# Kernel optimization log

Hardware: AMD Instinct MI355X
Metric: run time of the kernel (lower is better)

## Reference

```python
import jax, jax.numpy as jnp
import numpy as np

N = 100000          # nodes
E = 3200000         # edges (before self-loops)
F_IN = 745
HID = 128
N_CLS = 8
NEG_SLOPE = 0.2
EPS = 1e-16  # PyG softmax epsilon


def gat_conv(x, W, a_src, a_dst, b, src, dst):
    """Single-head GATConv (PyG semantics, self-loops already in src/dst)."""
    h = x @ W                                   # [N, out]
    s_src = h @ a_src                           # [N] per-node source logit
    s_dst = h @ a_dst                           # [N] per-node dest logit
    e = jax.nn.leaky_relu(s_src[src] + s_dst[dst], NEG_SLOPE)  # [E']
    # numerically stable per-destination softmax
    m = jax.ops.segment_max(e, dst, num_segments=N)
    e = jnp.exp(e - m[dst])
    denom = jax.ops.segment_sum(e, dst, num_segments=N)
    alpha = e / (denom[dst] + EPS)              # [E']
    out = jax.ops.segment_sum(alpha[:, None] * h[src], dst, num_segments=N)
    return out + b


def setup_inputs() -> dict:
    key = jax.random.key(0)
    ks = jax.random.split(key, 10)
    x = jax.random.normal(ks[0], (N, F_IN), dtype=jnp.float32)
    edge_index = jax.random.randint(ks[1], (2, E), 0, N, dtype=jnp.int64)
    # layer 1 params (Glorot-ish scale)
    W1 = jax.random.normal(ks[2], (F_IN, HID), dtype=jnp.float32) * (1.0 / np.sqrt(F_IN))
    a1_src = jax.random.normal(ks[3], (HID,), dtype=jnp.float32) * (1.0 / np.sqrt(HID))
    a1_dst = jax.random.normal(ks[4], (HID,), dtype=jnp.float32) * (1.0 / np.sqrt(HID))
    b1 = jnp.zeros((HID,), dtype=jnp.float32)
    # layer 2 params
    W2 = jax.random.normal(ks[5], (HID, N_CLS), dtype=jnp.float32) * (1.0 / np.sqrt(HID))
    a2_src = jax.random.normal(ks[6], (N_CLS,), dtype=jnp.float32) * (1.0 / np.sqrt(N_CLS))
    a2_dst = jax.random.normal(ks[7], (N_CLS,), dtype=jnp.float32) * (1.0 / np.sqrt(N_CLS))
    b2 = jnp.zeros((N_CLS,), dtype=jnp.float32)
    return {"x": x, "edge_index": edge_index, "W1": W1, "a1_src": a1_src,
            "a1_dst": a1_dst, "b1": b1, "W2": W2, "a2_src": a2_src,
            "a2_dst": a2_dst, "b2": b2}


def reference(x, edge_index, W1, a1_src, a1_dst, b1, W2, a2_src, a2_dst, b2):
    # add self-loops (PyG GATConv default add_self_loops=True)
    loop = jnp.arange(N, dtype=edge_index.dtype)
    src = jnp.concatenate([edge_index[0], loop])
    dst = jnp.concatenate([edge_index[1], loop])
    h = gat_conv(x, W1, a1_src, a1_dst, b1, src, dst)
    h = jax.nn.relu(h)
    # dropout p=0.5 is identity in eval mode
    out = gat_conv(h, W2, a2_src, a2_dst, b2, src, dst)
    return out
```

## Files before the change

### kernel.cpp

```cpp
#include <hip/hip_runtime.h>
#include <stdint.h>

#define NN 100000
#define EE 3200000
#define NEDGE (EE + NN)
#define KD 745
#define GKP 768
#define HD 128
#define NC 8

#define BS 256
#define NBK 391
#define NBLK 784
#define CHUNK ((NEDGE + NBLK - 1) / NBLK)

typedef unsigned short ushort_t;
typedef __attribute__((ext_vector_type(8))) short short8;
typedef __attribute__((ext_vector_type(4))) float f32x4;

__device__ __forceinline__ ushort_t f2bf(float f) {
  unsigned int u = __float_as_uint(f);
  u += 0x7FFFu + ((u >> 16) & 1u);
  return (ushort_t)(u >> 16);
}
__device__ __forceinline__ float bf2f(ushort_t h) {
  return __uint_as_float(((unsigned int)h) << 16);
}
__device__ __forceinline__ float lrelu_exp(float t) {
  return __expf(t >= 0.f ? t : 0.2f * t);
}

__global__ void k_detect(const int* __restrict__ ei, int* __restrict__ flag) {
  if (threadIdx.x == 0) {
    int orv = 0;
    #pragma unroll
    for (int i = 0; i < 16; i++) orv |= ei[2 * i + 1];
    flag[0] = (orv == 0) ? 1 : 0;
  }
}

__device__ __forceinline__ void edge_sd(const int* __restrict__ ei, int flag, int e,
                                        int& s, int& d) {
  if (e < EE) {
    if (flag) {
      s = ((const int2*)ei)[e].x;
      d = ((const int2*)ei)[EE + e].x;
    } else {
      s = ei[e];
      d = ei[EE + e];
    }
  } else { s = e - EE; d = s; }
}

__global__ __launch_bounds__(256)
void k_prepw1(const float* __restrict__ W1, ushort_t* __restrict__ WhiT,
              ushort_t* __restrict__ WloT) {
  int idx = blockIdx.x * 256 + threadIdx.x;
  if (idx >= HD * GKP) return;
  int n = idx / GKP, k = idx % GKP;
  float v = (k < KD) ? W1[(size_t)k * HD + n] : 0.f;
  ushort_t hi = f2bf(v);
  ushort_t lo = f2bf(v - bf2f(hi));
  WhiT[(size_t)n * GKP + k] = hi;
  WloT[(size_t)n * GKP + k] = lo;
}

__global__ __launch_bounds__(256, 2)
void k_gemm1(const float* __restrict__ x, const ushort_t* __restrict__ WhiT,
             const ushort_t* __restrict__ WloT, float* __restrict__ h1) {
  __shared__ ushort_t Ah[128 * 32], Al[128 * 32], Bh[128 * 32], Bl[128 * 32];
  const int tid = threadIdx.x;
  const int lane = tid & 63;
  const int wid = tid >> 6;
  const int wr = wid >> 1, wc = wid & 1;
  const long long row0 = (long long)blockIdx.x * 128;
  const int am = tid >> 1, ah = tid & 1;

  f32x4 acc[4][4];
  #pragma unroll
  for (int i = 0; i < 4; i++)
    #pragma unroll
    for (int j = 0; j < 4; j++) acc[i][j] = (f32x4){0.f, 0.f, 0.f, 0.f};

  for (int k0 = 0; k0 < GKP; k0 += 32) {
    {
      long long gr = row0 + am;
      int kb = k0 + ah * 16;
      float v[16];
      if (gr < NN && kb + 16 <= KD) {
        const float* xp = x + gr * KD + kb;
        #pragma unroll
        for (int i = 0; i < 16; i++) v[i] = xp[i];
      } else if (gr < NN) {
        const float* xp = x + gr * KD + kb;
        #pragma unroll
        for (int i = 0; i < 16; i++) v[i] = (kb + i < KD) ? xp[i] : 0.f;
      } else {
        #pragma unroll
        for (int i = 0; i < 16; i++) v[i] = 0.f;
      }
      ushort_t* ph = &Ah[am * 32 + ah * 16];
      ushort_t* pl = &Al[am * 32 + ah * 16];
      #pragma unroll
      for (int i = 0; i < 16; i++) {
        ushort_t hi = f2bf(v[i]);
        ph[i] = hi;
        pl[i] = f2bf(v[i] - bf2f(hi));
      }
    }
    {
      const int bn = tid >> 1, off = (tid & 1) * 16;
      const ushort_t* gh = WhiT + (size_t)bn * GKP + k0 + off;
      const ushort_t* gl = WloT + (size_t)bn * GKP + k0 + off;
      ushort_t* dh = &Bh[bn * 32 + off];
      ushort_t* dl = &Bl[bn * 32 + off];
      *(short8*)dh = *(const short8*)gh;
      *(short8*)(dh + 8) = *(const short8*)(gh + 8);
      *(short8*)dl = *(const short8*)gl;
      *(short8*)(dl + 8) = *(const short8*)(gl + 8);
    }
    __syncthreads();

    const int rr = lane & 15, kk = (lane >> 4) * 8;
    short8 a_h[4], a_l[4], b_h[4], b_l[4];
    #pragma unroll
    for (int i = 0; i < 4; i++) {
      a_h[i] = *(const short8*)&Ah[(wr * 64 + i * 16 + rr) * 32 + kk];
      a_l[i] = *(const short8*)&Al[(wr * 64 + i * 16 + rr) * 32 + kk];
      b_h[i] = *(const short8*)&Bh[(wc * 64 + i * 16 + rr) * 32 + kk];
      b_l[i] = *(const short8*)&Bl[(wc * 64 + i * 16 + rr) * 32 + kk];
    }
    #pragma unroll
    for (int i = 0; i < 4; i++)
      #pragma unroll
      for (int j = 0; j < 4; j++) {
        acc[i][j] = __builtin_amdgcn_mfma_f32_16x16x32_bf16(a_h[i], b_h[j], acc[i][j], 0, 0, 0);
        acc[i][j] = __builtin_amdgcn_mfma_f32_16x16x32_bf16(a_h[i], b_l[j], acc[i][j], 0, 0, 0);
        acc[i][j] = __builtin_amdgcn_mfma_f32_16x16x32_bf16(a_l[i], b_h[j], acc[i][j], 0, 0, 0);
      }
    __syncthreads();
  }
  #pragma unroll
  for (int i = 0; i < 4; i++)
    #pragma unroll
    for (int j = 0; j < 4; j++)
      #pragma unroll
      for (int r = 0; r < 4; r++) {
        long long grow = row0 + wr * 64 + i * 16 + (lane >> 4) * 4 + r;
        int gcol = wc * 64 + j * 16 + (lane & 15);
        if (grow < NN) h1[grow * HD + gcol] = acc[i][j][r];
      }
}

__global__ __launch_bounds__(256)
void k_s1(const float* __restrict__ h1, const float* __restrict__ as_,
          const float* __restrict__ ad_, float* __restrict__ s1s,
          float* __restrict__ s1d) {
  int w = threadIdx.x >> 6, lane = threadIdx.x & 63;
  int n = blockIdx.x * 4 + w;
  if (n >= NN) return;
  const float* hp = h1 + (size_t)n * HD;
  float h0 = hp[lane], h1v = hp[lane + 64];
  float ps = h0 * as_[lane] + h1v * as_[lane + 64];
  float pd = h0 * ad_[lane] + h1v * ad_[lane + 64];
  #pragma unroll
  for (int m = 32; m; m >>= 1) {
    ps += __shfl_xor(ps, m, 64);
    pd += __shfl_xor(pd, m, 64);
  }
  if (lane == 0) { s1s[n] = ps; s1d[n] = pd; }
}

__global__ __launch_bounds__(256)
void k_hist(const int* __restrict__ ei, const int* __restrict__ flagp,
            int* __restrict__ hist) {
  __shared__ int cnt[NBK];
  const int flag = flagp[0];
  int b = blockIdx.x, t = threadIdx.x;
  for (int i = t; i < NBK; i += 256) cnt[i] = 0;
  __syncthreads();
  int e0 = b * CHUNK;
  int e1 = e0 + CHUNK; if (e1 > NEDGE) e1 = NEDGE;
  for (int e = e0 + t; e < e1; e += 256) {
    int s, d;
    edge_sd(ei, flag, e, s, d);
    atomicAdd(&cnt[d >> 8], 1);
  }
  __syncthreads();
  for (int i = t; i < NBK; i += 256) hist[(size_t)i * NBLK + b] = cnt[i];
}

__global__ __launch_bounds__(256)
void k_scanA(int* __restrict__ hist, int* __restrict__ btot) {
  __shared__ int sm[1024];
  int j = blockIdx.x, t = threadIdx.x;
  #pragma unroll
  for (int c = 0; c < 4; c++) {
    int i = t + 256 * c;
    sm[i] = (i < NBLK) ? hist[(size_t)j * NBLK + i] : 0;
  }
  __syncthreads();
  for (int d = 1; d < 1024; d <<= 1) {
    int v[4];
    #pragma unroll
    for (int c = 0; c < 4; c++) {
      int i = t + 256 * c;
      v[c] = (i >= d) ? sm[i - d] : 0;
    }
    __syncthreads();
    #pragma unroll
    for (int c = 0; c < 4; c++) sm[t + 256 * c] += v[c];
    __syncthreads();
  }
  #pragma unroll
  for (int c = 0; c < 4; c++) {
    int i = t + 256 * c;
    if (i < NBLK) hist[(size_t)j * NBLK + i] = (i == 0) ? 0 : sm[i - 1];
  }
  if (t == 0) btot[j] = sm[NBLK - 1];
}

__global__ __launch_bounds__(256)
void k_bscan(const int* __restrict__ btot, int* __restrict__ bbase) {
  __shared__ int sm[512];
  int t = threadIdx.x;
  for (int i = t; i < 512; i += 256) sm[i] = (i < NBK) ? btot[i] : 0;
  __syncthreads();
  for (int d = 1; d < 512; d <<= 1) {
    int v0 = (t >= d) ? sm[t - d] : 0;
    int v1 = sm[t + 256 - d];
    __syncthreads();
    sm[t] += v0;
    sm[t + 256] += v1;
    __syncthreads();
  }
  for (int i = t; i <= NBK; i += 256) bbase[i] = (i == 0) ? 0 : sm[i - 1];
}

__global__ __launch_bounds__(256)
void k_place(const int* __restrict__ ei, const int* __restrict__ flagp,
             const int* __restrict__ hist, const int* __restrict__ bbase,
             int* __restrict__ pairs) {
  __shared__ int ofs[NBK];
  const int flag = flagp[0];
  int b = blockIdx.x, t = threadIdx.x;
  for (int i = t; i < NBK; i += 256)
    ofs[i] = bbase[i] + hist[(size_t)i * NBLK + b];
  __syncthreads();
  int e0 = b * CHUNK;
  int e1 = e0 + CHUNK; if (e1 > NEDGE) e1 = NEDGE;
  for (int e = e0 + t; e < e1; e += 256) {
    int s, d;
    edge_sd(ei, flag, e, s, d);
    int pos = atomicAdd(&ofs[d >> 8], 1);
    pairs[pos] = s | ((d & 255) << 17);
  }
}

__global__ __launch_bounds__(256)
void k_part2(const int* __restrict__ pairs, const int* __restrict__ bbase,
             int* __restrict__ rp, int* __restrict__ adj) {
  __shared__ int cnt[BS], fillv[BS], wsum[4];
  int b = blockIdx.x, t = threadIdx.x;
  int n0 = b * BS;
  int j0 = bbase[b];
  int ne = bbase[b + 1] - j0;
  const int* pb = pairs + j0;
  cnt[t] = 0;
  __syncthreads();
  for (int j = t; j < ne; j += 256)
    atomicAdd(&cnt[((unsigned)pb[j]) >> 17], 1);
  __syncthreads();
  int lane = t & 63, w = t >> 6;
  int v = cnt[t];
  int xv = v;
  #pragma unroll
  for (int d = 1; d < 64; d <<= 1) {
    int y = __shfl_up(xv, d, 64);
    if (lane >= d) xv += y;
  }
  if (lane == 63) wsum[w] = xv;
  __syncthreads();
  int woff = 0;
  #pragma unroll
  for (int i = 0; i < 4; i++) if (i < w) woff += wsum[i];
  int excl = j0 + woff + xv - v;
  if (n0 + t < NN) rp[n0 + t] = excl;
  fillv[t] = excl;
  __syncthreads();
  for (int j = t; j < ne; j += 256) {
    int p = pb[j];
    int pos = atomicAdd(&fillv[((unsigned)p) >> 17], 1);
    adj[pos] = p & 0x1FFFF;
  }
  if (b == 0 && t == 0) rp[NN] = NEDGE;
}

__global__ __launch_bounds__(256)
void k_agg1h2(const float* __restrict__ h1, const int* __restrict__ adj,
              const int* __restrict__ rp, const float* __restrict__ s1s,
              const float* __restrict__ s1d, const float* __restrict__ b1,
              const float* __restrict__ W2, const float* __restrict__ a2s,
              const float* __restrict__ a2d, float* __restrict__ h2,
              float* __restrict__ s2s, float* __restrict__ s2d) {
  __shared__ float W2T[NC * HD];
  int t = threadIdx.x;
  for (int i = t; i < HD * NC; i += 256) {
    int f = i >> 3, k = i & 7;
    W2T[k * HD + f] = W2[i];
  }
  __syncthreads();
  int wv = t >> 6, lane = t & 63;
  int n = blockIdx.x * 4 + wv;
  if (n >= NN) return;
  int half = lane >> 5, l32 = lane & 31;
  int j0 = rp[n], j1 = rp[n + 1];
  int deg = j1 - j0;
  int dh = (deg + 1) >> 1;
  int js = half ? (j0 + dh) : j0;
  int je = half ? j1 : (j0 + dh);
  float sdv = s1d[n];
  f32x4 acc = (f32x4){0.f, 0.f, 0.f, 0.f};
  float dsum = 0.f;
  int j = js;
  for (; j + 4 <= je; j += 4) {
    int e0 = adj[j], e1 = adj[j + 1], e2 = adj[j + 2], e3 = adj[j + 3];
    f32x4 v0 = *(const f32x4*)(h1 + (size_t)e0 * HD + l32 * 4);
    f32x4 v1 = *(const f32x4*)(h1 + (size_t)e1 * HD + l32 * 4);
    f32x4 v2 = *(const f32x4*)(h1 + (size_t)e2 * HD + l32 * 4);
    f32x4 v3 = *(const f32x4*)(h1 + (size_t)e3 * HD + l32 * 4);
    float w0 = lrelu_exp(s1s[e0] + sdv);
    float w1 = lrelu_exp(s1s[e1] + sdv);
    float w2 = lrelu_exp(s1s[e2] + sdv);
    float w3 = lrelu_exp(s1s[e3] + sdv);
    acc += w0 * v0; acc += w1 * v1; acc += w2 * v2; acc += w3 * v3;
    dsum += (w0 + w1) + (w2 + w3);
  }
  for (; j < je; ++j) {
    int e0 = adj[j];
    f32x4 v0 = *(const f32x4*)(h1 + (size_t)e0 * HD + l32 * 4);
    float w0 = lrelu_exp(s1s[e0] + sdv);
    acc += w0 * v0; dsum += w0;
  }
  #pragma unroll
  for (int c = 0; c < 4; c++) acc[c] += __shfl_xor(acc[c], 32, 64);
  dsum += __shfl_xor(dsum, 32, 64);
  float inv = 1.f / (dsum + 1e-16f);
  f32x4 bv = *(const f32x4*)(b1 + l32 * 4);
  f32x4 x2v;
  #pragma unroll
  for (int c = 0; c < 4; c++) {
    float r = acc[c] * inv + bv[c];
    x2v[c] = r > 0.f ? r : 0.f;
  }
  float hk[NC];
  #pragma unroll
  for (int k = 0; k < NC; k++) {
    f32x4 wv4 = *(const f32x4*)&W2T[k * HD + l32 * 4];
    hk[k] = x2v[0] * wv4[0] + x2v[1] * wv4[1] + x2v[2] * wv4[2] + x2v[3] * wv4[3];
  }
  #pragma unroll
  for (int m = 1; m < 32; m <<= 1)
    #pragma unroll
    for (int k = 0; k < NC; k++) hk[k] += __shfl_xor(hk[k], m, 64);
  if (lane == 0) {
    float ss = 0.f, sd = 0.f;
    #pragma unroll
    for (int k = 0; k < NC; k++) {
      h2[(size_t)n * NC + k] = hk[k];
      ss += hk[k] * a2s[k];
      sd += hk[k] * a2d[k];
    }
    s2s[n] = ss;
    s2d[n] = sd;
  }
}

__global__ __launch_bounds__(256)
void k_agg2(const float* __restrict__ h2, const int* __restrict__ adj,
            const int* __restrict__ rp, const float* __restrict__ s2s,
            const float* __restrict__ s2d, const float* __restrict__ b2,
            float* __restrict__ out) {
  int wv = threadIdx.x >> 6, lane = threadIdx.x & 63;
  int n = blockIdx.x * 4 + wv;
  if (n >= NN) return;
  int sub = lane >> 3, k = lane & 7;
  int j0 = rp[n], j1 = rp[n + 1];
  float sdv = s2d[n];
  float a = 0.f, dsum = 0.f;
  for (int j = j0 + sub; j < j1; j += 8) {
    int s = adj[j];
    float wvv = lrelu_exp(s2s[s] + sdv);
    a += wvv * h2[(size_t)s * NC + k];
    dsum += wvv;
  }
  #pragma unroll
  for (int m = 8; m < 64; m <<= 1) {
    a += __shfl_xor(a, m, 64);
    dsum += __shfl_xor(dsum, m, 64);
  }
  if (sub == 0) out[(size_t)n * NC + k] = a / (dsum + 1e-16f) + b2[k];
}

extern "C" void kernel_launch(void* const* d_in, const int* in_sizes, int n_in,
                              void* d_out, int out_size, void* d_ws, size_t ws_size,
                              hipStream_t stream) {
  (void)in_sizes; (void)n_in; (void)out_size;
  const float* x   = (const float*)d_in[0];
  const int*   ei  = (const int*)d_in[1];
  const float* W1  = (const float*)d_in[2];
  const float* a1s = (const float*)d_in[3];
  const float* a1d = (const float*)d_in[4];
  const float* b1  = (const float*)d_in[5];
  const float* W2  = (const float*)d_in[6];
  const float* a2s = (const float*)d_in[7];
  const float* a2d = (const float*)d_in[8];
  const float* b2  = (const float*)d_in[9];
  float* out = (float*)d_out;
  char* ws = (char*)d_ws;

  size_t o = 0;
  auto take = [&](size_t bytes) { size_t c = o; o += (bytes + 255) & ~(size_t)255; return c; };
  size_t o_flag  = take(64);
  size_t o_whi   = take((size_t)HD * GKP * 2);
  size_t o_wlo   = take((size_t)HD * GKP * 2);
  size_t o_h1    = take((size_t)NN * HD * 4);
  size_t o_h2    = take((size_t)NN * NC * 4);
  size_t o_s1s   = take((size_t)NN * 4);
  size_t o_s1d   = take((size_t)NN * 4);
  size_t o_s2s   = take((size_t)NN * 4);
  size_t o_s2d   = take((size_t)NN * 4);
  size_t o_rp    = take((size_t)(NN + 1) * 4);
  size_t o_adj   = take((size_t)NEDGE * 4);
  size_t o_pairs = take((size_t)NEDGE * 4);
  size_t o_hist  = take((size_t)NBK * NBLK * 4);
  size_t o_btot  = take((size_t)NBK * 4);
  size_t o_bbase = take((size_t)(NBK + 1) * 4);
  if (o > ws_size) return;

  int*   flag = (int*)(ws + o_flag);
  ushort_t* whi = (ushort_t*)(ws + o_whi);
  ushort_t* wlo = (ushort_t*)(ws + o_wlo);
  float* h1  = (float*)(ws + o_h1);
  float* h2  = (float*)(ws + o_h2);
  float* s1s = (float*)(ws + o_s1s);
  float* s1d = (float*)(ws + o_s1d);
  float* s2s = (float*)(ws + o_s2s);
  float* s2d = (float*)(ws + o_s2d);
  int* rp    = (int*)(ws + o_rp);
  int* adj   = (int*)(ws + o_adj);
  int* pairs = (int*)(ws + o_pairs);
  int* hist  = (int*)(ws + o_hist);
  int* btot  = (int*)(ws + o_btot);
  int* bbase = (int*)(ws + o_bbase);

  k_detect<<<1, 64, 0, stream>>>(ei, flag);
  k_prepw1<<<(HD * GKP + 255) / 256, 256, 0, stream>>>(W1, whi, wlo);
  k_gemm1<<<(NN + 127) / 128, 256, 0, stream>>>(x, whi, wlo, h1);
  k_s1<<<(NN + 3) / 4, 256, 0, stream>>>(h1, a1s, a1d, s1s, s1d);
  k_hist<<<NBLK, 256, 0, stream>>>(ei, flag, hist);
  k_scanA<<<NBK, 256, 0, stream>>>(hist, btot);
  k_bscan<<<1, 256, 0, stream>>>(btot, bbase);
  k_place<<<NBLK, 256, 0, stream>>>(ei, flag, hist, bbase, pairs);
  k_part2<<<NBK, 256, 0, stream>>>(pairs, bbase, rp, adj);
  k_agg1h2<<<(NN + 3) / 4, 256, 0, stream>>>(h1, adj, rp, s1s, s1d, b1, W2,
                                             a2s, a2d, h2, s2s, s2d);
  k_agg2<<<(NN + 3) / 4, 256, 0, stream>>>(h2, adj, rp, s2s, s2d, b2, out);
}
```

Baseline: 891.4 us.

## Store h1 as bf16, fuse attention logits into GEMM epilogue

```diff
diff --git a/kernel.cpp b/kernel.cpp
--- a/kernel.cpp
+++ b/kernel.cpp
@@ -8,6 +8,7 @@
 #define GKP 768
 #define HD 128
 #define NC 8
+#define HDP 132
 
 #define BS 256
 #define NBK 391
@@ -17,6 +18,7 @@
 typedef unsigned short ushort_t;
 typedef __attribute__((ext_vector_type(8))) short short8;
 typedef __attribute__((ext_vector_type(4))) float f32x4;
+typedef __attribute__((ext_vector_type(4))) ushort_t ushort4_t;
 
 __device__ __forceinline__ ushort_t f2bf(float f) {
   unsigned int u = __float_as_uint(f);
@@ -67,8 +69,11 @@
 
 __global__ __launch_bounds__(256, 2)
 void k_gemm1(const float* __restrict__ x, const ushort_t* __restrict__ WhiT,
-             const ushort_t* __restrict__ WloT, float* __restrict__ h1) {
+             const ushort_t* __restrict__ WloT, const float* __restrict__ a1s,
+             const float* __restrict__ a1d, ushort_t* __restrict__ h1b,
+             float* __restrict__ s1s, float* __restrict__ s1d) {
   __shared__ ushort_t Ah[128 * 32], Al[128 * 32], Bh[128 * 32], Bl[128 * 32];
+  __shared__ float sred[128][4];
   const int tid = threadIdx.x;
   const int lane = tid & 63;
   const int wid = tid >> 6;
@@ -140,35 +145,47 @@
       }
     __syncthreads();
   }
+
+  const int cl = lane & 15, gq = lane >> 4;
+  float avS[4], avD[4];
+  #pragma unroll
+  for (int j = 0; j < 4; j++) {
+    avS[j] = a1s[wc * 64 + j * 16 + cl];
+    avD[j] = a1d[wc * 64 + j * 16 + cl];
+  }
   #pragma unroll
   for (int i = 0; i < 4; i++)
     #pragma unroll
-    for (int j = 0; j < 4; j++)
+    for (int r = 0; r < 4; r++) {
+      long long grow = row0 + wr * 64 + i * 16 + gq * 4 + r;
+      float ps = 0.f, pd = 0.f;
       #pragma unroll
-      for (int r = 0; r < 4; r++) {
-        long long grow = row0 + wr * 64 + i * 16 + (lane >> 4) * 4 + r;
-        int gcol = wc * 64 + j * 16 + (lane & 15);
-        if (grow < NN) h1[grow * HD + gcol] = acc[i][j][r];
-      }
-}
-
-__global__ __launch_bounds__(256)
-void k_s1(const float* __restrict__ h1, const float* __restrict__ as_,
-          const float* __restrict__ ad_, float* __restrict__ s1s,
-          float* __restrict__ s1d) {
-  int w = threadIdx.x >> 6, lane = threadIdx.x & 63;
-  int n = blockIdx.x * 4 + w;
-  if (n >= NN) return;
-  const float* hp = h1 + (size_t)n * HD;
-  float h0 = hp[lane], h1v = hp[lane + 64];
-  float ps = h0 * as_[lane] + h1v * as_[lane + 64];
-  float pd = h0 * ad_[lane] + h1v * ad_[lane + 64];
-  #pragma unroll
-  for (int m = 32; m; m >>= 1) {
-    ps += __shfl_xor(ps, m, 64);
-    pd += __shfl_xor(pd, m, 64);
-  }
-  if (lane == 0) { s1s[n] = ps; s1d[n] = pd; }
+      for (int j = 0; j < 4; j++) {
+        float hv = acc[i][j][r];
+        ps += hv * avS[j];
+        pd += hv * avD[j];
+        if (grow < NN)
+          h1b[grow * HD + wc * 64 + j * 16 + cl] = f2bf(hv);
+      }
+      #pragma unroll
+      for (int m = 1; m < 16; m <<= 1) {
+        ps += __shfl_xor(ps, m, 64);
+        pd += __shfl_xor(pd, m, 64);
+      }
+      if (cl == 0) {
+        int lrow = wr * 64 + i * 16 + gq * 4 + r;
+        sred[lrow][wc] = ps;
+        sred[lrow][2 + wc] = pd;
+      }
+    }
+  __syncthreads();
+  if (tid < 128) {
+    long long grow = row0 + tid;
+    if (grow < NN) {
+      s1s[grow] = sred[tid][0] + sred[tid][1];
+      s1d[grow] = sred[tid][2] + sred[tid][3];
+    }
+  }
 }
 
 __global__ __launch_bounds__(256)
@@ -297,17 +314,17 @@
 }
 
 __global__ __launch_bounds__(256)
-void k_agg1h2(const float* __restrict__ h1, const int* __restrict__ adj,
+void k_agg1h2(const ushort_t* __restrict__ h1b, const int* __restrict__ adj,
               const int* __restrict__ rp, const float* __restrict__ s1s,
               const float* __restrict__ s1d, const float* __restrict__ b1,
               const float* __restrict__ W2, const float* __restrict__ a2s,
               const float* __restrict__ a2d, float* __restrict__ h2,
               float* __restrict__ s2s, float* __restrict__ s2d) {
-  __shared__ float W2T[NC * HD];
+  __shared__ float W2T[NC * HDP];
   int t = threadIdx.x;
   for (int i = t; i < HD * NC; i += 256) {
     int f = i >> 3, k = i & 7;
-    W2T[k * HD + f] = W2[i];
+    W2T[k * HDP + f] = W2[i];
   }
   __syncthreads();
   int wv = t >> 6, lane = t & 63;
@@ -323,24 +340,35 @@
   f32x4 acc = (f32x4){0.f, 0.f, 0.f, 0.f};
   float dsum = 0.f;
   int j = js;
-  for (; j + 4 <= je; j += 4) {
-    int e0 = adj[j], e1 = adj[j + 1], e2 = adj[j + 2], e3 = adj[j + 3];
-    f32x4 v0 = *(const f32x4*)(h1 + (size_t)e0 * HD + l32 * 4);
-    f32x4 v1 = *(const f32x4*)(h1 + (size_t)e1 * HD + l32 * 4);
-    f32x4 v2 = *(const f32x4*)(h1 + (size_t)e2 * HD + l32 * 4);
-    f32x4 v3 = *(const f32x4*)(h1 + (size_t)e3 * HD + l32 * 4);
-    float w0 = lrelu_exp(s1s[e0] + sdv);
-    float w1 = lrelu_exp(s1s[e1] + sdv);
-    float w2 = lrelu_exp(s1s[e2] + sdv);
-    float w3 = lrelu_exp(s1s[e3] + sdv);
-    acc += w0 * v0; acc += w1 * v1; acc += w2 * v2; acc += w3 * v3;
-    dsum += (w0 + w1) + (w2 + w3);
+  for (; j + 8 <= je; j += 8) {
+    int e[8];
+    ushort4_t u[8];
+    float w[8];
+    #pragma unroll
+    for (int q = 0; q < 8; q++) e[q] = adj[j + q];
+    #pragma unroll
+    for (int q = 0; q < 8; q++)
+      u[q] = *(const ushort4_t*)(h1b + (size_t)e[q] * HD + l32 * 4);
+    #pragma unroll
+    for (int q = 0; q < 8; q++) w[q] = lrelu_exp(s1s[e[q]] + sdv);
+    #pragma unroll
+    for (int q = 0; q < 8; q++) {
+      acc[0] += w[q] * bf2f(u[q][0]);
+      acc[1] += w[q] * bf2f(u[q][1]);
+      acc[2] += w[q] * bf2f(u[q][2]);
+      acc[3] += w[q] * bf2f(u[q][3]);
+      dsum += w[q];
+    }
   }
   for (; j < je; ++j) {
     int e0 = adj[j];
-    f32x4 v0 = *(const f32x4*)(h1 + (size_t)e0 * HD + l32 * 4);
+    ushort4_t u = *(const ushort4_t*)(h1b + (size_t)e0 * HD + l32 * 4);
     float w0 = lrelu_exp(s1s[e0] + sdv);
-    acc += w0 * v0; dsum += w0;
+    acc[0] += w0 * bf2f(u[0]);
+    acc[1] += w0 * bf2f(u[1]);
+    acc[2] += w0 * bf2f(u[2]);
+    acc[3] += w0 * bf2f(u[3]);
+    dsum += w0;
   }
   #pragma unroll
   for (int c = 0; c < 4; c++) acc[c] += __shfl_xor(acc[c], 32, 64);
@@ -356,8 +384,8 @@
   float hk[NC];
   #pragma unroll
   for (int k = 0; k < NC; k++) {
-    f32x4 wv4 = *(const f32x4*)&W2T[k * HD + l32 * 4];
-    hk[k] = x2v[0] * wv4[0] + x2v[1] * wv4[1] + x2v[2] * wv4[2] + x2v[3] * wv4[3];
+    const float* wp = &W2T[k * HDP + l32 * 4];
+    hk[k] = x2v[0] * wp[0] + x2v[1] * wp[1] + x2v[2] * wp[2] + x2v[3] * wp[3];
   }
   #pragma unroll
   for (int m = 1; m < 32; m <<= 1)
@@ -424,7 +452,7 @@
   size_t o_flag  = take(64);
   size_t o_whi   = take((size_t)HD * GKP * 2);
   size_t o_wlo   = take((size_t)HD * GKP * 2);
-  size_t o_h1    = take((size_t)NN * HD * 4);
+  size_t o_h1    = take((size_t)NN * HD * 2);
   size_t o_h2    = take((size_t)NN * NC * 4);
   size_t o_s1s   = take((size_t)NN * 4);
   size_t o_s1d   = take((size_t)NN * 4);
@@ -441,7 +469,7 @@
   int*   flag = (int*)(ws + o_flag);
   ushort_t* whi = (ushort_t*)(ws + o_whi);
   ushort_t* wlo = (ushort_t*)(ws + o_wlo);
-  float* h1  = (float*)(ws + o_h1);
+  ushort_t* h1b = (ushort_t*)(ws + o_h1);
   float* h2  = (float*)(ws + o_h2);
   float* s1s = (float*)(ws + o_s1s);
   float* s1d = (float*)(ws + o_s1d);
@@ -456,14 +484,13 @@
 
   k_detect<<<1, 64, 0, stream>>>(ei, flag);
   k_prepw1<<<(HD * GKP + 255) / 256, 256, 0, stream>>>(W1, whi, wlo);
-  k_gemm1<<<(NN + 127) / 128, 256, 0, stream>>>(x, whi, wlo, h1);
-  k_s1<<<(NN + 3) / 4, 256, 0, stream>>>(h1, a1s, a1d, s1s, s1d);
+  k_gemm1<<<(NN + 127) / 128, 256, 0, stream>>>(x, whi, wlo, a1s, a1d, h1b, s1s, s1d);
   k_hist<<<NBLK, 256, 0, stream>>>(ei, flag, hist);
   k_scanA<<<NBK, 256, 0, stream>>>(hist, btot);
   k_bscan<<<1, 256, 0, stream>>>(btot, bbase);
   k_place<<<NBLK, 256, 0, stream>>>(ei, flag, hist, bbase, pairs);
   k_part2<<<NBK, 256, 0, stream>>>(pairs, bbase, rp, adj);
-  k_agg1h2<<<(NN + 3) / 4, 256, 0, stream>>>(h1, adj, rp, s1s, s1d, b1, W2,
+  k_agg1h2<<<(NN + 3) / 4, 256, 0, stream>>>(h1b, adj, rp, s1s, s1d, b1, W2,
                                              a2s, a2d, h2, s2s, s2d);
   k_agg2<<<(NN + 3) / 4, 256, 0, stream>>>(h2, adj, rp, s2s, s2d, b2, out);
 }
```

After: 791.6 us. -11.2%, faster.
